# Performance work log

Measured on AMD Instinct MI355X. Metric: run time of the kernel, lower is better.

## Reference

```python
import jax, jax.numpy as jnp
import numpy as np

B = 64
C = 12        # num_classes
NC = 16       # num_clusters
N0, N1, N2, N3, NDIM = 2048, 1000, 500, 100, 3
E = C * NC    # 192 residual heads


def _init(key, shape, fan_in):
    return jax.random.normal(key, shape, dtype=jnp.float32) / np.sqrt(fan_in)


def setup_inputs() -> dict:
    key = jax.random.key(0)
    ks = jax.random.split(key, 12)
    x = jax.random.normal(ks[0], (B, N0), dtype=jnp.float32)
    class_label = jax.random.randint(ks[1], (B, 1), 0, C)
    return {
        'x': x,
        'class_label': class_label,
        # bin_3layer weights, stacked over the class axis
        'W1b': _init(ks[2], (C, N1, N0), N0),
        'b1b': jnp.zeros((C, N1), jnp.float32),
        'W2b': _init(ks[3], (C, N2, N1), N1),
        'b2b': jnp.zeros((C, N2), jnp.float32),
        'W3b': _init(ks[4], (C, NC, N2), N2),
        'b3b': jnp.zeros((C, NC), jnp.float32),
        # res_2layer weights, stacked over class*cluster axis
        'W1r': _init(ks[5], (E, N3, N0), N0),
        'b1r': jnp.zeros((E, N3), jnp.float32),
        'W2r': _init(ks[6], (E, NDIM, N3), N3),
        'b2r': jnp.zeros((E, NDIM), jnp.float32),
    }


def reference(x, class_label, W1b, b1b, W2b, b2b, W3b, b3b, W1r, b1r, W2r, b2r):
    # --- bin heads: all classes computed (as the torch loop does), grouped GEMMs ---
    h = jax.nn.relu(jnp.einsum('bi,cji->bcj', x, W1b) + b1b)        # [B,C,N1]
    h = jax.nn.relu(jnp.einsum('bcj,ckj->bck', h, W2b) + b2b)       # [B,C,N2]
    y1_all = jnp.einsum('bck,cmk->bcm', h, W3b) + b3b               # [B,C,NC]

    # --- res heads: all class*cluster experts computed ---
    r = jax.nn.relu(jnp.einsum('bi,eji->bej', x, W1r) + b1r)        # [B,E,N3]
    y2_all = jnp.einsum('bej,edj->bed', r, W2r) + b2r               # [B,E,NDIM]
    y2_all = y2_all.reshape(B, C, NC, NDIM)

    # one-hot bmm over class axis == gather per-sample class
    cl = class_label[:, 0]                                           # [B]
    y1 = jnp.take_along_axis(y1_all, cl[:, None, None], axis=1)[:, 0]        # [B,NC]
    y2c = jnp.take_along_axis(y2_all, cl[:, None, None, None], axis=1)[:, 0] # [B,NC,NDIM]

    # argmax over clusters, then one-hot bmm over cluster axis == gather
    pose = jnp.argmax(y1, axis=1)                                    # [B]
    y2 = jnp.take_along_axis(y2c, pose[:, None, None], axis=1)[:, 0] # [B,NDIM]
    return y1, y2
```

## Files before the change

### kernel.cpp

```cpp
#include <hip/hip_runtime.h>

#define B_   64
#define C_   12
#define NC_  16
#define N0_  2048
#define N1_  1000
#define N2_  500
#define N3_  100

__device__ __forceinline__ float wred(float v) {
#pragma unroll
    for (int off = 32; off > 0; off >>= 1) v += __shfl_xor(v, off, 64);
    return v;
}

__global__ __launch_bounds__(256)
void k_l1b(const float* __restrict__ x, const int* __restrict__ cls,
           const float* __restrict__ W1b, const float* __restrict__ b1b,
           float* __restrict__ h1) {
    const int c    = blockIdx.y;
    const int lane = threadIdx.x & 63;
    const int wave = threadIdx.x >> 6;
    const unsigned long long m = __ballot(cls[lane] == c);
    if (m == 0ull) return;

    const int j0 = blockIdx.x * 8 + wave * 2;
    const float4* wr0 = (const float4*)(W1b + ((size_t)c * N1_ + j0) * N0_);
    const float4* wr1 = wr0 + (N0_ / 4);
    float4 w0[8], w1[8];
#pragma unroll
    for (int f = 0; f < 8; ++f) { w0[f] = wr0[f * 64 + lane]; w1[f] = wr1[f * 64 + lane]; }
    const float bias0 = b1b[c * N1_ + j0];
    const float bias1 = b1b[c * N1_ + j0 + 1];

    for (unsigned long long mm = m; mm; mm &= (mm - 1ull)) {
        const int b = (int)__builtin_ctzll(mm);
        const float4* xr = (const float4*)(x + (size_t)b * N0_);
        float a0 = 0.f, a1 = 0.f;
#pragma unroll
        for (int f = 0; f < 8; ++f) {
            const float4 xv = xr[f * 64 + lane];
            a0 += w0[f].x * xv.x + w0[f].y * xv.y + w0[f].z * xv.z + w0[f].w * xv.w;
            a1 += w1[f].x * xv.x + w1[f].y * xv.y + w1[f].z * xv.z + w1[f].w * xv.w;
        }
        const float s0 = wred(a0), s1 = wred(a1);
        if (lane == 0) {
            h1[(size_t)b * N1_ + j0]     = fmaxf(s0 + bias0, 0.f);
            h1[(size_t)b * N1_ + j0 + 1] = fmaxf(s1 + bias1, 0.f);
        }
    }
}

__global__ __launch_bounds__(1024)
void k_perb(const float* __restrict__ x, const int* __restrict__ cls,
            const float* __restrict__ h1,
            const float* __restrict__ W2b, const float* __restrict__ b2b,
            const float* __restrict__ W3b, const float* __restrict__ b3b,
            const float* __restrict__ W1r, const float* __restrict__ b1r,
            const float* __restrict__ W2r, const float* __restrict__ b2r,
            float* __restrict__ out_y1, float* __restrict__ out_y2) {
    const int b    = blockIdx.x;
    const int tid  = threadIdx.x;
    const int lane = tid & 63;
    const int wave = tid >> 6;
    const int c    = cls[b];

    __shared__ float s_x[N0_];
    __shared__ float s_h1[N1_];
    __shared__ float s_h2[N2_];
    __shared__ float s_y1[NC_];
    __shared__ float s_r[N3_];
    __shared__ int   s_e;

    for (int i = tid; i < N0_; i += 1024) s_x[i]  = x[(size_t)b * N0_ + i];
    for (int i = tid; i < N1_; i += 1024) s_h1[i] = h1[(size_t)b * N1_ + i];
    __syncthreads();

    {
        const float4 z4 = make_float4(0.f, 0.f, 0.f, 0.f);
        const float4* xr = (const float4*)s_h1;
        for (int j0 = wave * 2; j0 < N2_; j0 += 32) {
            const float4* wr0 = (const float4*)(W2b + ((size_t)c * N2_ + j0) * N1_);
            const float4* wr1 = wr0 + (N1_ / 4);
            float a0 = 0.f, a1 = 0.f;
#pragma unroll
            for (int f = 0; f < 4; ++f) {
                const int idx = f * 64 + lane;
                if (idx < N1_ / 4) {
                    const float4 xv = xr[idx];
                    const float4 w0 = wr0[idx], w1 = wr1[idx];
                    a0 += w0.x * xv.x + w0.y * xv.y + w0.z * xv.z + w0.w * xv.w;
                    a1 += w1.x * xv.x + w1.y * xv.y + w1.z * xv.z + w1.w * xv.w;
                }
            }
            const float s0 = wred(a0), s1 = wred(a1);
            if (lane == 0) {
                s_h2[j0]     = fmaxf(s0 + b2b[c * N2_ + j0],     0.f);
                s_h2[j0 + 1] = fmaxf(s1 + b2b[c * N2_ + j0 + 1], 0.f);
            }
        }
    }
    __syncthreads();

    if (wave < NC_) {
        const float* wrow = W3b + ((size_t)c * NC_ + wave) * N2_;
        float a = 0.f;
        for (int k = lane; k < N2_; k += 64) a += s_h2[k] * wrow[k];
        const float s = wred(a) + b3b[c * NC_ + wave];
        if (lane == 0) { s_y1[wave] = s; out_y1[b * NC_ + wave] = s; }
    }
    __syncthreads();

    if (wave == 0) {
        float v  = (lane < NC_) ? s_y1[lane] : -1e30f;
        int   mi = lane;
#pragma unroll
        for (int off = 8; off > 0; off >>= 1) {
            const float ov = __shfl_xor(v,  off, 16);
            const int   om = __shfl_xor(mi, off, 16);
            if (ov > v || (ov == v && om < mi)) { v = ov; mi = om; }
        }
        if (lane == 0) s_e = c * NC_ + mi;
    }
    __syncthreads();
    const int e = s_e;

    {
        const float4* xr = (const float4*)s_x;
        for (int j0 = wave * 2; j0 < N3_; j0 += 32) {
            const float4* wr0 = (const float4*)(W1r + ((size_t)e * N3_ + j0) * N0_);
            const float4* wr1 = wr0 + (N0_ / 4);
            float a0 = 0.f, a1 = 0.f;
#pragma unroll
            for (int f = 0; f < 8; ++f) {
                const int idx = f * 64 + lane;
                const float4 xv = xr[idx];
                const float4 w0 = wr0[idx], w1 = wr1[idx];
                a0 += w0.x * xv.x + w0.y * xv.y + w0.z * xv.z + w0.w * xv.w;
                a1 += w1.x * xv.x + w1.y * xv.y + w1.z * xv.z + w1.w * xv.w;
            }
            const float s0 = wred(a0), s1 = wred(a1);
            if (lane == 0) {
                s_r[j0]     = fmaxf(s0 + b1r[e * N3_ + j0],     0.f);
                s_r[j0 + 1] = fmaxf(s1 + b1r[e * N3_ + j0 + 1], 0.f);
            }
        }
    }
    __syncthreads();

    if (wave < 3) {
        const float* w2 = W2r + ((size_t)e * 3 + wave) * N3_;
        float a = s_r[lane] * w2[lane];
        if (lane < N3_ - 64) a += s_r[64 + lane] * w2[64 + lane];
        const float s = wred(a);
        if (lane == 0) out_y2[b * 3 + wave] = s + b2r[e * 3 + wave];
    }
}

extern "C" void kernel_launch(void* const* d_in, const int* in_sizes, int n_in,
                              void* d_out, int out_size, void* d_ws, size_t ws_size,
                              hipStream_t stream) {
    const float* x   = (const float*)d_in[0];
    const int*   cls = (const int*)  d_in[1];
    const float* W1b = (const float*)d_in[2];
    const float* b1b = (const float*)d_in[3];
    const float* W2b = (const float*)d_in[4];
    const float* b2b = (const float*)d_in[5];
    const float* W3b = (const float*)d_in[6];
    const float* b3b = (const float*)d_in[7];
    const float* W1r = (const float*)d_in[8];
    const float* b1r = (const float*)d_in[9];
    const float* W2r = (const float*)d_in[10];
    const float* b2r = (const float*)d_in[11];

    float* out_y1 = (float*)d_out;
    float* out_y2 = (float*)d_out + B_ * NC_;
    float* h1     = (float*)d_ws;

    hipLaunchKernelGGL(k_l1b, dim3(125, 12), dim3(256), 0, stream,
                       x, cls, W1b, b1b, h1);
    hipLaunchKernelGGL(k_perb, dim3(64), dim3(1024), 0, stream,
                       x, cls, h1, W2b, b2b, W3b, b3b, W1r, b1r, W2r, b2r,
                       out_y1, out_y2);
}
```

Before: 66.57 us.

## Split per-sample tail across four blocks with atomic reduction and flag handoff

The per-sample kernel is spread over four blocks per sample instead of one, each handling an interleaved quarter of the layer-2 rows and residual rows. The L3 matvec is fused into the L2 loop, and partial results are combined through global atomics. A last-arriver counter computes the argmax and publishes the chosen expert through a spin-waited flag. The layer-1 kernel now has each wave compute four output rows with float4 stores and also zeroes the accumulators. The aim is to raise occupancy in the latency-bound tail, at the cost of atomics and an inter-block spin wait that assumes all four blocks are co-resident.

Result: slower. 73.12 us (+9.8%).

```diff
diff --git a/kernel.cpp b/kernel.cpp
--- a/kernel.cpp
+++ b/kernel.cpp
@@ -7,6 +7,7 @@
 #define N1_  1000
 #define N2_  500
 #define N3_  100
+#define AGENT __HIP_MEMORY_SCOPE_AGENT
 
 __device__ __forceinline__ float wred(float v) {
 #pragma unroll
@@ -17,36 +18,49 @@
 __global__ __launch_bounds__(256)
 void k_l1b(const float* __restrict__ x, const int* __restrict__ cls,
            const float* __restrict__ W1b, const float* __restrict__ b1b,
-           float* __restrict__ h1) {
+           float* __restrict__ h1, int* __restrict__ zbase) {
+    if (blockIdx.x == 0 && blockIdx.y == 0) {
+        for (int i = threadIdx.x; i < 1408; i += 256) zbase[i] = 0;
+    }
     const int c    = blockIdx.y;
     const int lane = threadIdx.x & 63;
     const int wave = threadIdx.x >> 6;
     const unsigned long long m = __ballot(cls[lane] == c);
     if (m == 0ull) return;
 
-    const int j0 = blockIdx.x * 8 + wave * 2;
-    const float4* wr0 = (const float4*)(W1b + ((size_t)c * N1_ + j0) * N0_);
-    const float4* wr1 = wr0 + (N0_ / 4);
-    float4 w0[8], w1[8];
-#pragma unroll
-    for (int f = 0; f < 8; ++f) { w0[f] = wr0[f * 64 + lane]; w1[f] = wr1[f * 64 + lane]; }
-    const float bias0 = b1b[c * N1_ + j0];
-    const float bias1 = b1b[c * N1_ + j0 + 1];
+    const int j0 = blockIdx.x * 16 + wave * 4;
+    if (j0 >= N1_) return;
+
+    const float* wbase = W1b + ((size_t)c * N1_ + j0) * N0_;
+    float4 w[4][8];
+#pragma unroll
+    for (int k = 0; k < 4; ++k) {
+        const float4* wr = (const float4*)(wbase + (size_t)k * N0_);
+#pragma unroll
+        for (int f = 0; f < 8; ++f) w[k][f] = wr[f * 64 + lane];
+    }
+    const float4 bias = *(const float4*)(b1b + c * N1_ + j0);
 
     for (unsigned long long mm = m; mm; mm &= (mm - 1ull)) {
         const int b = (int)__builtin_ctzll(mm);
         const float4* xr = (const float4*)(x + (size_t)b * N0_);
-        float a0 = 0.f, a1 = 0.f;
+        float a0 = 0.f, a1 = 0.f, a2 = 0.f, a3 = 0.f;
 #pragma unroll
         for (int f = 0; f < 8; ++f) {
             const float4 xv = xr[f * 64 + lane];
-            a0 += w0[f].x * xv.x + w0[f].y * xv.y + w0[f].z * xv.z + w0[f].w * xv.w;
-            a1 += w1[f].x * xv.x + w1[f].y * xv.y + w1[f].z * xv.z + w1[f].w * xv.w;
-        }
-        const float s0 = wred(a0), s1 = wred(a1);
+            a0 += w[0][f].x * xv.x + w[0][f].y * xv.y + w[0][f].z * xv.z + w[0][f].w * xv.w;
+            a1 += w[1][f].x * xv.x + w[1][f].y * xv.y + w[1][f].z * xv.z + w[1][f].w * xv.w;
+            a2 += w[2][f].x * xv.x + w[2][f].y * xv.y + w[2][f].z * xv.z + w[2][f].w * xv.w;
+            a3 += w[3][f].x * xv.x + w[3][f].y * xv.y + w[3][f].z * xv.z + w[3][f].w * xv.w;
+        }
+        const float s0 = wred(a0), s1 = wred(a1), s2 = wred(a2), s3 = wred(a3);
         if (lane == 0) {
-            h1[(size_t)b * N1_ + j0]     = fmaxf(s0 + bias0, 0.f);
-            h1[(size_t)b * N1_ + j0 + 1] = fmaxf(s1 + bias1, 0.f);
+            float4 hv;
+            hv.x = fmaxf(s0 + bias.x, 0.f);
+            hv.y = fmaxf(s1 + bias.y, 0.f);
+            hv.z = fmaxf(s2 + bias.z, 0.f);
+            hv.w = fmaxf(s3 + bias.w, 0.f);
+            *(float4*)(h1 + (size_t)b * N1_ + j0) = hv;
         }
     }
 }
@@ -58,102 +72,121 @@
             const float* __restrict__ W3b, const float* __restrict__ b3b,
             const float* __restrict__ W1r, const float* __restrict__ b1r,
             const float* __restrict__ W2r, const float* __restrict__ b2r,
+            float* __restrict__ y1acc, int* __restrict__ cntb,
+            int* __restrict__ flag,  int* __restrict__ cnt2,
+            float* __restrict__ y2acc,
             float* __restrict__ out_y1, float* __restrict__ out_y2) {
-    const int b    = blockIdx.x;
+    const int b    = blockIdx.x >> 2;
+    const int q    = blockIdx.x & 3;
     const int tid  = threadIdx.x;
     const int lane = tid & 63;
     const int wave = tid >> 6;
     const int c    = cls[b];
 
-    __shared__ float s_x[N0_];
-    __shared__ float s_h1[N1_];
-    __shared__ float s_h2[N2_];
-    __shared__ float s_y1[NC_];
-    __shared__ float s_r[N3_];
+    __shared__ __align__(16) float s_x[N0_];
+    __shared__ __align__(16) float s_h1[N1_];
+    __shared__ float s_part[16][16];
     __shared__ int   s_e;
 
-    for (int i = tid; i < N0_; i += 1024) s_x[i]  = x[(size_t)b * N0_ + i];
-    for (int i = tid; i < N1_; i += 1024) s_h1[i] = h1[(size_t)b * N1_ + i];
-    __syncthreads();
-
     {
-        const float4 z4 = make_float4(0.f, 0.f, 0.f, 0.f);
+        const float4* xs = (const float4*)(x  + (size_t)b * N0_);
+        const float4* hs = (const float4*)(h1 + (size_t)b * N1_);
+        float4* xd = (float4*)s_x;
+        float4* hd = (float4*)s_h1;
+        if (tid < 512) xd[tid] = xs[tid];
+        else if (tid < 512 + 250) hd[tid - 512] = hs[tid - 512];
+    }
+    __syncthreads();
+
+    float accm = 0.f;
+    for (int idx = wave; idx < 125; idx += 16) {
+        const int j = 4 * idx + q;
+        const float4* wr = (const float4*)(W2b + ((size_t)c * N2_ + j) * N1_);
         const float4* xr = (const float4*)s_h1;
-        for (int j0 = wave * 2; j0 < N2_; j0 += 32) {
-            const float4* wr0 = (const float4*)(W2b + ((size_t)c * N2_ + j0) * N1_);
-            const float4* wr1 = wr0 + (N1_ / 4);
-            float a0 = 0.f, a1 = 0.f;
-#pragma unroll
-            for (int f = 0; f < 4; ++f) {
-                const int idx = f * 64 + lane;
-                if (idx < N1_ / 4) {
-                    const float4 xv = xr[idx];
-                    const float4 w0 = wr0[idx], w1 = wr1[idx];
-                    a0 += w0.x * xv.x + w0.y * xv.y + w0.z * xv.z + w0.w * xv.w;
-                    a1 += w1.x * xv.x + w1.y * xv.y + w1.z * xv.z + w1.w * xv.w;
-                }
+        float a = 0.f;
+#pragma unroll
+        for (int f = 0; f < 4; ++f) {
+            const int id4 = f * 64 + lane;
+            if (id4 < N1_ / 4) {
+                const float4 wv = wr[id4], xv = xr[id4];
+                a += wv.x * xv.x + wv.y * xv.y + wv.z * xv.z + wv.w * xv.w;
             }
-            const float s0 = wred(a0), s1 = wred(a1);
-            if (lane == 0) {
-                s_h2[j0]     = fmaxf(s0 + b2b[c * N2_ + j0],     0.f);
-                s_h2[j0 + 1] = fmaxf(s1 + b2b[c * N2_ + j0 + 1], 0.f);
+        }
+        const float h2v = fmaxf(wred(a) + b2b[c * N2_ + j], 0.f);
+        if (lane < NC_) accm += h2v * W3b[((size_t)c * NC_ + lane) * N2_ + j];
+    }
+    if (lane < NC_) s_part[wave][lane] = accm;
+    __syncthreads();
+
+    if (wave == 0) {
+        if (lane < NC_) {
+            float t = 0.f;
+#pragma unroll
+            for (int w = 0; w < 16; ++w) t += s_part[w][lane];
+            __hip_atomic_fetch_add(&y1acc[b * NC_ + lane], t, __ATOMIC_RELAXED, AGENT);
+        }
+        int old = 0;
+        if (lane == 0) old = __hip_atomic_fetch_add(&cntb[b], 1, __ATOMIC_ACQ_REL, AGENT);
+        old = __shfl(old, 0, 64);
+        if (old == 3) {
+            float v = -1e30f;
+            if (lane < NC_) {
+                v = __hip_atomic_load(&y1acc[b * NC_ + lane], __ATOMIC_RELAXED, AGENT)
+                    + b3b[c * NC_ + lane];
+                out_y1[b * NC_ + lane] = v;
             }
-        }
-    }
-    __syncthreads();
-
-    if (wave < NC_) {
-        const float* wrow = W3b + ((size_t)c * NC_ + wave) * N2_;
+            int mi = lane;
+#pragma unroll
+            for (int off = 8; off > 0; off >>= 1) {
+                const float ov = __shfl_xor(v,  off, 16);
+                const int   om = __shfl_xor(mi, off, 16);
+                if (ov > v || (ov == v && om < mi)) { v = ov; mi = om; }
+            }
+            if (lane == 0)
+                __hip_atomic_store(&flag[b], 1 + c * NC_ + mi, __ATOMIC_RELEASE, AGENT);
+        }
+        int fv = 0;
+        if (lane == 0) {
+            while ((fv = __hip_atomic_load(&flag[b], __ATOMIC_RELAXED, AGENT)) == 0)
+                __builtin_amdgcn_s_sleep(1);
+            s_e = fv - 1;
+        }
+    }
+    __syncthreads();
+    const int e = s_e;
+
+    float y2p = 0.f;
+    for (int idx = wave; idx < 25; idx += 16) {
+        const int j = 4 * idx + q;
+        const float4* wr = (const float4*)(W1r + ((size_t)e * N3_ + j) * N0_);
+        const float4* xr = (const float4*)s_x;
         float a = 0.f;
-        for (int k = lane; k < N2_; k += 64) a += s_h2[k] * wrow[k];
-        const float s = wred(a) + b3b[c * NC_ + wave];
-        if (lane == 0) { s_y1[wave] = s; out_y1[b * NC_ + wave] = s; }
-    }
+#pragma unroll
+        for (int f = 0; f < 8; ++f) {
+            const int id4 = f * 64 + lane;
+            const float4 wv = wr[id4], xv = xr[id4];
+            a += wv.x * xv.x + wv.y * xv.y + wv.z * xv.z + wv.w * xv.w;
+        }
+        const float rv = fmaxf(wred(a) + b1r[e * N3_ + j], 0.f);
+        if (lane < 3) y2p += rv * W2r[((size_t)e * 3 + lane) * N3_ + j];
+    }
+    if (lane < NC_) s_part[wave][lane] = (lane < 3) ? y2p : 0.f;
     __syncthreads();
 
     if (wave == 0) {
-        float v  = (lane < NC_) ? s_y1[lane] : -1e30f;
-        int   mi = lane;
-#pragma unroll
-        for (int off = 8; off > 0; off >>= 1) {
-            const float ov = __shfl_xor(v,  off, 16);
-            const int   om = __shfl_xor(mi, off, 16);
-            if (ov > v || (ov == v && om < mi)) { v = ov; mi = om; }
-        }
-        if (lane == 0) s_e = c * NC_ + mi;
-    }
-    __syncthreads();
-    const int e = s_e;
-
-    {
-        const float4* xr = (const float4*)s_x;
-        for (int j0 = wave * 2; j0 < N3_; j0 += 32) {
-            const float4* wr0 = (const float4*)(W1r + ((size_t)e * N3_ + j0) * N0_);
-            const float4* wr1 = wr0 + (N0_ / 4);
-            float a0 = 0.f, a1 = 0.f;
-#pragma unroll
-            for (int f = 0; f < 8; ++f) {
-                const int idx = f * 64 + lane;
-                const float4 xv = xr[idx];
-                const float4 w0 = wr0[idx], w1 = wr1[idx];
-                a0 += w0.x * xv.x + w0.y * xv.y + w0.z * xv.z + w0.w * xv.w;
-                a1 += w1.x * xv.x + w1.y * xv.y + w1.z * xv.z + w1.w * xv.w;
-            }
-            const float s0 = wred(a0), s1 = wred(a1);
-            if (lane == 0) {
-                s_r[j0]     = fmaxf(s0 + b1r[e * N3_ + j0],     0.f);
-                s_r[j0 + 1] = fmaxf(s1 + b1r[e * N3_ + j0 + 1], 0.f);
-            }
-        }
-    }
-    __syncthreads();
-
-    if (wave < 3) {
-        const float* w2 = W2r + ((size_t)e * 3 + wave) * N3_;
-        float a = s_r[lane] * w2[lane];
-        if (lane < N3_ - 64) a += s_r[64 + lane] * w2[64 + lane];
-        const float s = wred(a);
-        if (lane == 0) out_y2[b * 3 + wave] = s + b2r[e * 3 + wave];
+        if (lane < 3) {
+            float t = 0.f;
+#pragma unroll
+            for (int w = 0; w < 16; ++w) t += s_part[w][lane];
+            __hip_atomic_fetch_add(&y2acc[b * 3 + lane], t, __ATOMIC_RELAXED, AGENT);
+        }
+        int old = 0;
+        if (lane == 0) old = __hip_atomic_fetch_add(&cnt2[b], 1, __ATOMIC_ACQ_REL, AGENT);
+        old = __shfl(old, 0, 64);
+        if (old == 3 && lane < 3) {
+            const float vv = __hip_atomic_load(&y2acc[b * 3 + lane], __ATOMIC_RELAXED, AGENT);
+            out_y2[b * 3 + lane] = vv + b2r[e * 3 + lane];
+        }
     }
 }
 
@@ -175,11 +208,19 @@
 
     float* out_y1 = (float*)d_out;
     float* out_y2 = (float*)d_out + B_ * NC_;
-    float* h1     = (float*)d_ws;
-
-    hipLaunchKernelGGL(k_l1b, dim3(125, 12), dim3(256), 0, stream,
-                       x, cls, W1b, b1b, h1);
-    hipLaunchKernelGGL(k_perb, dim3(64), dim3(1024), 0, stream,
+
+    char*  ws    = (char*)d_ws;
+    float* h1    = (float*)(ws);
+    float* y1acc = (float*)(ws + 256000);
+    int*   cntb  = (int*)  (ws + 260096);
+    int*   flag  = (int*)  (ws + 260352);
+    int*   cnt2  = (int*)  (ws + 260608);
+    float* y2acc = (float*)(ws + 260864);
+    int*   zbase = (int*)  (ws + 256000);
+
+    hipLaunchKernelGGL(k_l1b, dim3(63, 12), dim3(256), 0, stream,
+                       x, cls, W1b, b1b, h1, zbase);
+    hipLaunchKernelGGL(k_perb, dim3(256), dim3(1024), 0, stream,
                        x, cls, h1, W2b, b2b, W3b, b3b, W1r, b1r, W2r, b2r,
-                       out_y1, out_y2);
-}
+                       y1acc, cntb, flag, cnt2, y2acc, out_y1, out_y2);
+}
```

## Replace per-sample tail kernel with class-grouped layer-2 and flag-synchronised residual split

Applied to the files above, without the earlier changes.

Splits the second stage into 256 blocks. 192 of them compute layer 2 grouped by class, reusing each weight row across every sample of that class instead of reloading it once per sample. The other 64 blocks wait on an atomic counter, then compute layer 3 and the argmax per sample and publish the chosen expert through a flag. The residual layer-1 work is split four ways per sample with cross-block partial sums and a last-arriver reduction. This cuts redundant W2b traffic and raises parallelism over the old 64-block tail. In exchange it relies on spin-waits that need all 256 blocks to be co-resident, plus extra atomics and global round trips.

Measured after the change: 86.22 us. +29.5%, slower.

```diff
diff --git a/kernel.cpp b/kernel.cpp
--- a/kernel.cpp
+++ b/kernel.cpp
@@ -7,6 +7,7 @@
 #define N1_  1000
 #define N2_  500
 #define N3_  100
+#define AGENT __HIP_MEMORY_SCOPE_AGENT
 
 __device__ __forceinline__ float wred(float v) {
 #pragma unroll
@@ -17,7 +18,10 @@
 __global__ __launch_bounds__(256)
 void k_l1b(const float* __restrict__ x, const int* __restrict__ cls,
            const float* __restrict__ W1b, const float* __restrict__ b1b,
-           float* __restrict__ h1) {
+           float* __restrict__ h1, int* __restrict__ zctrl) {
+    if (blockIdx.x == 0 && blockIdx.y == 0) {
+        for (int i = threadIdx.x; i < 2064; i += 256) zctrl[i] = 0;
+    }
     const int c    = blockIdx.y;
     const int lane = threadIdx.x & 63;
     const int wave = threadIdx.x >> 6;
@@ -51,109 +55,157 @@
     }
 }
 
-__global__ __launch_bounds__(1024)
-void k_perb(const float* __restrict__ x, const int* __restrict__ cls,
-            const float* __restrict__ h1,
+__global__ __launch_bounds__(256)
+void k_tail(const float* __restrict__ x, const int* __restrict__ cls,
+            const float* __restrict__ h1, float* __restrict__ h2,
             const float* __restrict__ W2b, const float* __restrict__ b2b,
             const float* __restrict__ W3b, const float* __restrict__ b3b,
             const float* __restrict__ W1r, const float* __restrict__ b1r,
             const float* __restrict__ W2r, const float* __restrict__ b2r,
+            int* __restrict__ zctrl, float* __restrict__ y2part,
             float* __restrict__ out_y1, float* __restrict__ out_y2) {
-    const int b    = blockIdx.x;
     const int tid  = threadIdx.x;
     const int lane = tid & 63;
     const int wave = tid >> 6;
-    const int c    = cls[b];
-
-    __shared__ float s_x[N0_];
-    __shared__ float s_h1[N1_];
+    const int blk  = blockIdx.x;
+
+    int* doneL2 = zctrl;
+    int* flag   = zctrl + 16;
+    int* cnt2   = zctrl + 1040;
+
+    __shared__ __align__(16) float s_x[N0_];
     __shared__ float s_h2[N2_];
     __shared__ float s_y1[NC_];
-    __shared__ float s_r[N3_];
+    __shared__ float s_part[4][3];
     __shared__ int   s_e;
 
-    for (int i = tid; i < N0_; i += 1024) s_x[i]  = x[(size_t)b * N0_ + i];
-    for (int i = tid; i < N1_; i += 1024) s_h1[i] = h1[(size_t)b * N1_ + i];
-    __syncthreads();
-
-    {
+    int b, q;
+    if (blk < 192) {
+        const int cls_lane = cls[lane];
         const float4 z4 = make_float4(0.f, 0.f, 0.f, 0.f);
-        const float4* xr = (const float4*)s_h1;
-        for (int j0 = wave * 2; j0 < N2_; j0 += 32) {
+        for (int t = blk * 4 + wave; t < C_ * (N2_ / 2); t += 768) {
+            const int c  = t / (N2_ / 2);
+            const int j0 = (t % (N2_ / 2)) * 2;
+            const unsigned long long m = __ballot(cls_lane == c);
+            if (m == 0ull) continue;
             const float4* wr0 = (const float4*)(W2b + ((size_t)c * N2_ + j0) * N1_);
             const float4* wr1 = wr0 + (N1_ / 4);
-            float a0 = 0.f, a1 = 0.f;
+            float4 w0[4], w1[4];
 #pragma unroll
             for (int f = 0; f < 4; ++f) {
                 const int idx = f * 64 + lane;
-                if (idx < N1_ / 4) {
-                    const float4 xv = xr[idx];
-                    const float4 w0 = wr0[idx], w1 = wr1[idx];
-                    a0 += w0.x * xv.x + w0.y * xv.y + w0.z * xv.z + w0.w * xv.w;
-                    a1 += w1.x * xv.x + w1.y * xv.y + w1.z * xv.z + w1.w * xv.w;
+                const bool v = (idx < N1_ / 4);
+                w0[f] = v ? wr0[idx] : z4;
+                w1[f] = v ? wr1[idx] : z4;
+            }
+            const float bias0 = b2b[c * N2_ + j0];
+            const float bias1 = b2b[c * N2_ + j0 + 1];
+            for (unsigned long long mm = m; mm; mm &= (mm - 1ull)) {
+                const int bb = (int)__builtin_ctzll(mm);
+                const float4* xr = (const float4*)(h1 + (size_t)bb * N1_);
+                float a0 = 0.f, a1 = 0.f;
+#pragma unroll
+                for (int f = 0; f < 4; ++f) {
+                    const int idx = f * 64 + lane;
+                    const float4 xv = (idx < N1_ / 4) ? xr[idx] : z4;
+                    a0 += w0[f].x * xv.x + w0[f].y * xv.y + w0[f].z * xv.z + w0[f].w * xv.w;
+                    a1 += w1[f].x * xv.x + w1[f].y * xv.y + w1[f].z * xv.z + w1[f].w * xv.w;
                 }
-            }
-            const float s0 = wred(a0), s1 = wred(a1);
-            if (lane == 0) {
-                s_h2[j0]     = fmaxf(s0 + b2b[c * N2_ + j0],     0.f);
-                s_h2[j0 + 1] = fmaxf(s1 + b2b[c * N2_ + j0 + 1], 0.f);
-            }
-        }
-    }
+                const float s0 = wred(a0), s1 = wred(a1);
+                if (lane == 0) {
+                    h2[(size_t)bb * N2_ + j0]     = fmaxf(s0 + bias0, 0.f);
+                    h2[(size_t)bb * N2_ + j0 + 1] = fmaxf(s1 + bias1, 0.f);
+                }
+            }
+        }
+        __syncthreads();
+        if (tid == 0) {
+            __threadfence();
+            __hip_atomic_fetch_add(doneL2, 1, __ATOMIC_ACQ_REL, AGENT);
+        }
+        b = blk / 3;  q = (blk % 3) + 1;
+        for (int i = tid; i < N0_ / 4; i += 256)
+            ((float4*)s_x)[i] = ((const float4*)(x + (size_t)b * N0_))[i];
+        if (tid == 0) {
+            int fv;
+            while ((fv = __hip_atomic_load(&flag[b * 16], __ATOMIC_RELAXED, AGENT)) == 0)
+                __builtin_amdgcn_s_sleep(1);
+            s_e = fv - 1;
+        }
+        __syncthreads();
+    } else {
+        b = blk - 192;  q = 0;
+        for (int i = tid; i < N0_ / 4; i += 256)
+            ((float4*)s_x)[i] = ((const float4*)(x + (size_t)b * N0_))[i];
+        if (tid == 0) {
+            while (__hip_atomic_load(doneL2, __ATOMIC_RELAXED, AGENT) < 192)
+                __builtin_amdgcn_s_sleep(2);
+            __hip_atomic_fetch_add(doneL2, 0, __ATOMIC_ACQ_REL, AGENT);
+        }
+        __syncthreads();
+        for (int i = tid; i < N2_; i += 256) s_h2[i] = h2[(size_t)b * N2_ + i];
+        __syncthreads();
+
+        const int c = cls[b];
+        for (int mi = wave; mi < NC_; mi += 4) {
+            const float* wrow = W3b + ((size_t)c * NC_ + mi) * N2_;
+            float a = 0.f;
+            for (int k = lane; k < N2_; k += 64) a += s_h2[k] * wrow[k];
+            const float s = wred(a) + b3b[c * NC_ + mi];
+            if (lane == 0) { s_y1[mi] = s; out_y1[b * NC_ + mi] = s; }
+        }
+        __syncthreads();
+        if (wave == 0) {
+            float v  = (lane < NC_) ? s_y1[lane] : -1e30f;
+            int   mi = lane;
+#pragma unroll
+            for (int off = 8; off > 0; off >>= 1) {
+                const float ov = __shfl_xor(v,  off, 16);
+                const int   om = __shfl_xor(mi, off, 16);
+                if (ov > v || (ov == v && om < mi)) { v = ov; mi = om; }
+            }
+            if (lane == 0) s_e = c * NC_ + mi;
+        }
+        __syncthreads();
+        if (tid == 0)
+            __hip_atomic_store(&flag[b * 16], 1 + s_e, __ATOMIC_RELEASE, AGENT);
+    }
+
+    const int e = s_e;
+    float y2p = 0.f;
+    for (int idx = wave; idx < 25; idx += 4) {
+        const int j = 4 * idx + q;
+        const float4* wr = (const float4*)(W1r + ((size_t)e * N3_ + j) * N0_);
+        const float4* xr = (const float4*)s_x;
+        float a = 0.f;
+#pragma unroll
+        for (int f = 0; f < 8; ++f) {
+            const int id = f * 64 + lane;
+            const float4 wv = wr[id], xv = xr[id];
+            a += wv.x * xv.x + wv.y * xv.y + wv.z * xv.z + wv.w * xv.w;
+        }
+        const float rv = fmaxf(wred(a) + b1r[e * N3_ + j], 0.f);
+        if (lane < 3) y2p += rv * W2r[((size_t)e * 3 + lane) * N3_ + j];
+    }
+    if (lane < 3) s_part[wave][lane] = y2p;
     __syncthreads();
-
-    if (wave < NC_) {
-        const float* wrow = W3b + ((size_t)c * NC_ + wave) * N2_;
-        float a = 0.f;
-        for (int k = lane; k < N2_; k += 64) a += s_h2[k] * wrow[k];
-        const float s = wred(a) + b3b[c * NC_ + wave];
-        if (lane == 0) { s_y1[wave] = s; out_y1[b * NC_ + wave] = s; }
+    if (tid < 3) {
+        const float t4 = s_part[0][tid] + s_part[1][tid] + s_part[2][tid] + s_part[3][tid];
+        y2part[(size_t)(b * 4 + q) * 4 + tid] = t4;
     }
     __syncthreads();
-
-    if (wave == 0) {
-        float v  = (lane < NC_) ? s_y1[lane] : -1e30f;
-        int   mi = lane;
-#pragma unroll
-        for (int off = 8; off > 0; off >>= 1) {
-            const float ov = __shfl_xor(v,  off, 16);
-            const int   om = __shfl_xor(mi, off, 16);
-            if (ov > v || (ov == v && om < mi)) { v = ov; mi = om; }
-        }
-        if (lane == 0) s_e = c * NC_ + mi;
-    }
-    __syncthreads();
-    const int e = s_e;
-
-    {
-        const float4* xr = (const float4*)s_x;
-        for (int j0 = wave * 2; j0 < N3_; j0 += 32) {
-            const float4* wr0 = (const float4*)(W1r + ((size_t)e * N3_ + j0) * N0_);
-            const float4* wr1 = wr0 + (N0_ / 4);
-            float a0 = 0.f, a1 = 0.f;
-#pragma unroll
-            for (int f = 0; f < 8; ++f) {
-                const int idx = f * 64 + lane;
-                const float4 xv = xr[idx];
-                const float4 w0 = wr0[idx], w1 = wr1[idx];
-                a0 += w0.x * xv.x + w0.y * xv.y + w0.z * xv.z + w0.w * xv.w;
-                a1 += w1.x * xv.x + w1.y * xv.y + w1.z * xv.z + w1.w * xv.w;
-            }
-            const float s0 = wred(a0), s1 = wred(a1);
-            if (lane == 0) {
-                s_r[j0]     = fmaxf(s0 + b1r[e * N3_ + j0],     0.f);
-                s_r[j0 + 1] = fmaxf(s1 + b1r[e * N3_ + j0 + 1], 0.f);
-            }
-        }
-    }
-    __syncthreads();
-
-    if (wave < 3) {
-        const float* w2 = W2r + ((size_t)e * 3 + wave) * N3_;
-        float a = s_r[lane] * w2[lane];
-        if (lane < N3_ - 64) a += s_r[64 + lane] * w2[64 + lane];
-        const float s = wred(a);
-        if (lane == 0) out_y2[b * 3 + wave] = s + b2r[e * 3 + wave];
+    if (tid == 0) {
+        __threadfence();
+        const int old = __hip_atomic_fetch_add(&cnt2[b * 16], 1, __ATOMIC_ACQ_REL, AGENT);
+        if (old == 3) {
+#pragma unroll
+            for (int d = 0; d < 3; ++d) {
+                float t5 = b2r[e * 3 + d];
+#pragma unroll
+                for (int qq = 0; qq < 4; ++qq) t5 += y2part[(size_t)(b * 4 + qq) * 4 + d];
+                out_y2[b * 3 + d] = t5;
+            }
+        }
     }
 }
 
@@ -175,11 +227,16 @@
 
     float* out_y1 = (float*)d_out;
     float* out_y2 = (float*)d_out + B_ * NC_;
-    float* h1     = (float*)d_ws;
+
+    char*  ws     = (char*)d_ws;
+    float* h1     = (float*)(ws);
+    float* h2     = (float*)(ws + 256000);
+    int*   zctrl  = (int*)  (ws + 384000);
+    float* y2part = (float*)(ws + 392256);
 
     hipLaunchKernelGGL(k_l1b, dim3(125, 12), dim3(256), 0, stream,
-                       x, cls, W1b, b1b, h1);
-    hipLaunchKernelGGL(k_perb, dim3(64), dim3(1024), 0, stream,
-                       x, cls, h1, W2b, b2b, W3b, b3b, W1r, b1r, W2r, b2r,
-                       out_y1, out_y2);
-}
+                       x, cls, W1b, b1b, h1, zctrl);
+    hipLaunchKernelGGL(k_tail, dim3(256), dim3(256), 0, stream,
+                       x, cls, h1, h2, W2b, b2b, W3b, b3b, W1r, b1r, W2r, b2r,
+                       zctrl, y2part, out_y1, out_y2);
+}
```

## Split per-sample layer-2 work across four blocks with atomic y1 reduction

Applied to the files above, without the earlier changes.

The per-sample kernel now launches four blocks per sample, each computing an interleaved quarter of the 500 layer-2 outputs. Each block folds its outputs directly into partial layer-3 logits using a staged slice of W3b, so the h2 buffer and a barrier are no longer needed. Partials are accumulated into a global buffer with atomics, and a counter picks the last-arriving block to run argmax and the residual head. The first kernel zeroes the accumulator and counter. This raises parallelism from 64 blocks to 256, at the cost of atomics, a fence, and a serialized tail in one block per sample.

After: 59.58 us. 1.12x faster.

```diff
diff --git a/kernel.cpp b/kernel.cpp
--- a/kernel.cpp
+++ b/kernel.cpp
@@ -7,6 +7,7 @@
 #define N1_  1000
 #define N2_  500
 #define N3_  100
+#define AGENT __HIP_MEMORY_SCOPE_AGENT
 
 __device__ __forceinline__ float wred(float v) {
 #pragma unroll
@@ -17,7 +18,10 @@
 __global__ __launch_bounds__(256)
 void k_l1b(const float* __restrict__ x, const int* __restrict__ cls,
            const float* __restrict__ W1b, const float* __restrict__ b1b,
-           float* __restrict__ h1) {
+           float* __restrict__ h1, int* __restrict__ zctrl) {
+    if (blockIdx.x == 0 && blockIdx.y == 0) {
+        for (int i = threadIdx.x; i < 2048; i += 256) zctrl[i] = 0;
+    }
     const int c    = blockIdx.y;
     const int lane = threadIdx.x & 63;
     const int wave = threadIdx.x >> 6;
@@ -52,68 +56,78 @@
 }
 
 __global__ __launch_bounds__(1024)
-void k_perb(const float* __restrict__ x, const int* __restrict__ cls,
-            const float* __restrict__ h1,
-            const float* __restrict__ W2b, const float* __restrict__ b2b,
-            const float* __restrict__ W3b, const float* __restrict__ b3b,
-            const float* __restrict__ W1r, const float* __restrict__ b1r,
-            const float* __restrict__ W2r, const float* __restrict__ b2r,
-            float* __restrict__ out_y1, float* __restrict__ out_y2) {
-    const int b    = blockIdx.x;
+void k_perb2(const float* __restrict__ x, const int* __restrict__ cls,
+             const float* __restrict__ h1,
+             const float* __restrict__ W2b, const float* __restrict__ b2b,
+             const float* __restrict__ W3b, const float* __restrict__ b3b,
+             const float* __restrict__ W1r, const float* __restrict__ b1r,
+             const float* __restrict__ W2r, const float* __restrict__ b2r,
+             float* __restrict__ y1acc, int* __restrict__ cnt,
+             float* __restrict__ out_y1, float* __restrict__ out_y2) {
+    const int b    = blockIdx.x >> 2;
+    const int q    = blockIdx.x & 3;
     const int tid  = threadIdx.x;
     const int lane = tid & 63;
     const int wave = tid >> 6;
     const int c    = cls[b];
 
-    __shared__ float s_x[N0_];
-    __shared__ float s_h1[N1_];
-    __shared__ float s_h2[N2_];
-    __shared__ float s_y1[NC_];
+    __shared__ __align__(16) float s_h1[N1_];
+    __shared__ float s_w3[NC_][125];
+    __shared__ float s_part[16][NC_];
+    __shared__ __align__(16) float s_x[N0_];
     __shared__ float s_r[N3_];
+    __shared__ int   s_old;
     __shared__ int   s_e;
 
-    for (int i = tid; i < N0_; i += 1024) s_x[i]  = x[(size_t)b * N0_ + i];
-    for (int i = tid; i < N1_; i += 1024) s_h1[i] = h1[(size_t)b * N1_ + i];
-    __syncthreads();
-
-    {
-        const float4 z4 = make_float4(0.f, 0.f, 0.f, 0.f);
+    if (tid < 250) ((float4*)s_h1)[tid] = ((const float4*)(h1 + (size_t)b * N1_))[tid];
+    for (int i = tid; i < NC_ * 125; i += 1024) {
+        const int mi = i / 125, idx = i - mi * 125;
+        s_w3[mi][idx] = W3b[((size_t)c * NC_ + mi) * N2_ + 4 * idx + q];
+    }
+    __syncthreads();
+
+    float accm = 0.f;
+    for (int idx = wave; idx < 125; idx += 16) {
+        const int j = 4 * idx + q;
+        const float4* wr = (const float4*)(W2b + ((size_t)c * N2_ + j) * N1_);
         const float4* xr = (const float4*)s_h1;
-        for (int j0 = wave * 2; j0 < N2_; j0 += 32) {
-            const float4* wr0 = (const float4*)(W2b + ((size_t)c * N2_ + j0) * N1_);
-            const float4* wr1 = wr0 + (N1_ / 4);
-            float a0 = 0.f, a1 = 0.f;
-#pragma unroll
-            for (int f = 0; f < 4; ++f) {
-                const int idx = f * 64 + lane;
-                if (idx < N1_ / 4) {
-                    const float4 xv = xr[idx];
-                    const float4 w0 = wr0[idx], w1 = wr1[idx];
-                    a0 += w0.x * xv.x + w0.y * xv.y + w0.z * xv.z + w0.w * xv.w;
-                    a1 += w1.x * xv.x + w1.y * xv.y + w1.z * xv.z + w1.w * xv.w;
-                }
+        float a = 0.f;
+#pragma unroll
+        for (int f = 0; f < 4; ++f) {
+            const int id4 = f * 64 + lane;
+            if (id4 < N1_ / 4) {
+                const float4 wv = wr[id4], xv = xr[id4];
+                a += wv.x * xv.x + wv.y * xv.y + wv.z * xv.z + wv.w * xv.w;
             }
-            const float s0 = wred(a0), s1 = wred(a1);
-            if (lane == 0) {
-                s_h2[j0]     = fmaxf(s0 + b2b[c * N2_ + j0],     0.f);
-                s_h2[j0 + 1] = fmaxf(s1 + b2b[c * N2_ + j0 + 1], 0.f);
-            }
-        }
-    }
-    __syncthreads();
-
-    if (wave < NC_) {
-        const float* wrow = W3b + ((size_t)c * NC_ + wave) * N2_;
-        float a = 0.f;
-        for (int k = lane; k < N2_; k += 64) a += s_h2[k] * wrow[k];
-        const float s = wred(a) + b3b[c * NC_ + wave];
-        if (lane == 0) { s_y1[wave] = s; out_y1[b * NC_ + wave] = s; }
-    }
-    __syncthreads();
+        }
+        const float h2v = fmaxf(wred(a) + b2b[c * N2_ + j], 0.f);
+        if (lane < NC_) accm += h2v * s_w3[lane][idx];
+    }
+    if (lane < NC_) s_part[wave][lane] = accm;
+    __syncthreads();
+
+    if (wave == 0 && lane < NC_) {
+        float t = 0.f;
+#pragma unroll
+        for (int w = 0; w < 16; ++w) t += s_part[w][lane];
+        __hip_atomic_fetch_add(&y1acc[b * NC_ + lane], t, __ATOMIC_RELAXED, AGENT);
+    }
+    if (tid == 0) {
+        __threadfence();
+        s_old = __hip_atomic_fetch_add(&cnt[b * 16], 1, __ATOMIC_ACQ_REL, AGENT);
+    }
+    __syncthreads();
+    if (s_old != 3) return;
+
+    if (tid < 512) ((float4*)s_x)[tid] = ((const float4*)(x + (size_t)b * N0_))[tid];
 
     if (wave == 0) {
-        float v  = (lane < NC_) ? s_y1[lane] : -1e30f;
+        float v  = -1e30f;
         int   mi = lane;
+        if (lane < NC_) {
+            v = y1acc[b * NC_ + lane] + b3b[c * NC_ + lane];
+            out_y1[b * NC_ + lane] = v;
+        }
 #pragma unroll
         for (int off = 8; off > 0; off >>= 1) {
             const float ov = __shfl_xor(v,  off, 16);
@@ -175,11 +189,16 @@
 
     float* out_y1 = (float*)d_out;
     float* out_y2 = (float*)d_out + B_ * NC_;
-    float* h1     = (float*)d_ws;
+
+    char*  ws    = (char*)d_ws;
+    float* h1    = (float*)(ws);
+    float* y1acc = (float*)(ws + 256000);
+    int*   cnt   = (int*)  (ws + 260096);
+    int*   zctrl = (int*)  (ws + 256000);
 
     hipLaunchKernelGGL(k_l1b, dim3(125, 12), dim3(256), 0, stream,
-                       x, cls, W1b, b1b, h1);
-    hipLaunchKernelGGL(k_perb, dim3(64), dim3(1024), 0, stream,
+                       x, cls, W1b, b1b, h1, zctrl);
+    hipLaunchKernelGGL(k_perb2, dim3(256), dim3(1024), 0, stream,
                        x, cls, h1, W2b, b2b, W3b, b3b, W1r, b1r, W2r, b2r,
-                       out_y1, out_y2);
-}
+                       y1acc, cnt, out_y1, out_y2);
+}
```
